# Kernel tuning notes

Hardware: AMD Instinct MI355X
Metric: run time of the kernel (lower is better)

Reference implementation:

```python
import jax, jax.numpy as jnp
import numpy as np

N = 50000      # nodes
E = 800000     # edges (avg degree 16)
IN_F = 128
HID = 128
NCLS = 64


def _lin(k, fi, fo):
    return jax.random.normal(k, (fi, fo), dtype=jnp.float32) / np.float32(np.sqrt(fi))


def setup_inputs() -> dict:
    key = jax.random.key(0)
    ks = jax.random.split(key, 10)
    features = jax.random.normal(ks[0], (N, IN_F), dtype=jnp.float32)
    noise = jax.random.normal(ks[1], (N, HID), dtype=jnp.float32)
    edge_src = jax.random.randint(ks[2], (E,), 0, N, dtype=jnp.int32)
    edge_dst = jax.random.randint(ks[3], (E,), 0, N, dtype=jnp.int32)
    Ws0 = _lin(ks[4], IN_F, HID); Wn0 = _lin(ks[5], IN_F, HID); b0 = jnp.zeros((HID,), jnp.float32)
    Ws1 = _lin(ks[6], HID, HID);  Wn1 = _lin(ks[7], HID, HID);  b1 = jnp.zeros((HID,), jnp.float32)
    Ws2 = _lin(ks[8], HID, NCLS); Wn2 = _lin(ks[9], HID, NCLS); b2 = jnp.zeros((NCLS,), jnp.float32)
    return dict(features=features, noise=noise,
                Ws0=Ws0, Wn0=Wn0, b0=b0,
                Ws1=Ws1, Wn1=Wn1, b1=b1,
                Ws2=Ws2, Wn2=Wn2, b2=b2,
                edge_src=edge_src, edge_dst=edge_dst, noise_d=1)


def _sage_layer(h, Ws, Wn, b, act, edge_src, edge_dst, deg_inv):
    # mean aggregation over incoming neighbors: gather src feats, segment-sum by dst
    msum = jax.ops.segment_sum(h[edge_src], edge_dst, num_segments=N)  # [N, F]
    h_neigh = msum * deg_inv[:, None]
    out = h @ Ws + h_neigh @ Wn + b
    return jax.nn.relu(out) if act else out


def reference(features, noise, Ws0, Wn0, b0, Ws1, Wn1, b1, Ws2, Wn2, b2,
              edge_src, edge_dst, noise_d):
    deg = jax.ops.segment_sum(jnp.ones((E,), jnp.float32), edge_dst, num_segments=N)
    deg_inv = 1.0 / jnp.maximum(deg, 1.0)
    layers = [(Ws0, Wn0, b0, True), (Ws1, Wn1, b1, True), (Ws2, Wn2, b2, False)]
    h = features
    h_noise = h
    for i, (Ws, Wn, b, act) in enumerate(layers):
        h = _sage_layer(h, Ws, Wn, b, act, edge_src, edge_dst, deg_inv)
        if noise_d == i:
            h_noise = h + noise
        if noise_d < i:
            h_noise = _sage_layer(h_noise, Ws, Wn, b, act, edge_src, edge_dst, deg_inv)
    return jnp.concatenate((h_noise, h), axis=1)  # [N, 2*NCLS]
```

## Files before the change

### kernel.cpp

```cpp
#include <hip/hip_runtime.h>

typedef __attribute__((ext_vector_type(8))) short bf16x8;
typedef __attribute__((ext_vector_type(4))) float f32x4;
typedef __attribute__((ext_vector_type(2))) float f32x2;

__device__ __forceinline__ unsigned short f2bf(float x) {
    union { float f; unsigned u; } v; v.f = x;
    unsigned r = v.u + 0x7FFFu + ((v.u >> 16) & 1u);
    return (unsigned short)(r >> 16);
}
__device__ __forceinline__ float bf2f(unsigned u) {
    union { unsigned u; float f; } v; v.u = u << 16;
    return v.f;
}
__device__ __forceinline__ unsigned char f2fp8(float x) {
    return (unsigned char)(__builtin_amdgcn_cvt_pk_fp8_f32(x, x, 0, false) & 0xff);
}

#define CHUNK 4096
#define CAP 4608

__global__ __launch_bounds__(256) void k_wt(
    const float* __restrict__ Ws0, const float* __restrict__ Wn0,
    const float* __restrict__ Ws1, const float* __restrict__ Wn1,
    const float* __restrict__ Ws2, const float* __restrict__ Wn2,
    unsigned short* __restrict__ WT0s, unsigned short* __restrict__ WT0n,
    unsigned short* __restrict__ WT1s, unsigned short* __restrict__ WT1n,
    unsigned short* __restrict__ WT2, int* __restrict__ bcursor) {
    int tid = threadIdx.x;
    if (blockIdx.x == 0) bcursor[tid] = 0;
    int i = blockIdx.x * 256 + tid;
    if (i < 16384)      { int j = i;         WT0s[j] = f2bf(Ws0[(j & 127) * 128 + (j >> 7)]); }
    else if (i < 32768) { int j = i - 16384; WT0n[j] = f2bf(Wn0[(j & 127) * 128 + (j >> 7)]); }
    else if (i < 49152) { int j = i - 32768; WT1s[j] = f2bf(Ws1[(j & 127) * 128 + (j >> 7)]); }
    else if (i < 65536) { int j = i - 49152; WT1n[j] = f2bf(Wn1[(j & 127) * 128 + (j >> 7)]); }
    else if (i < 73728) { int j = i - 65536; WT2[j] = f2bf(Ws2[(j & 127) * 64 + (j >> 7)]); }
    else if (i < 81920) { int j = i - 73728; WT2[8192 + j] = f2bf(Wn2[(j & 127) * 64 + (j >> 7)]); }
}

__global__ __launch_bounds__(256) void k_scatter_gemm0(
    const int* __restrict__ esrc, const int* __restrict__ edst,
    int* __restrict__ bcursor, unsigned* __restrict__ bsorted, int E, int ech,
    const float* __restrict__ Xf,
    const unsigned short* __restrict__ WsT, const unsigned short* __restrict__ WnT,
    const float* __restrict__ bias, unsigned short* __restrict__ Ab,
    unsigned char* __restrict__ T8, int N) {
    __shared__ uint4 smem[1216];
    int tid = threadIdx.x;
    if ((int)blockIdx.x < ech) {
        unsigned* stage = (unsigned*)smem;
        int* hist = (int*)(stage + CHUNK);
        int* base = hist + 256;
        int* cur  = base + 256;
        hist[tid] = 0;
        __syncthreads();
        int e0 = blockIdx.x * CHUNK;
        int cnt = min(CHUNK, E - e0);
        for (int i = tid; i < cnt; i += 256) {
            int d = edst[e0 + i], s = esrc[e0 + i];
            stage[i] = ((unsigned)d << 16) | (unsigned)s;
            atomicAdd(&hist[d >> 8], 1);
        }
        __syncthreads();
        int h = hist[tid];
        base[tid] = h ? (tid * CAP + atomicAdd(&bcursor[tid], h)) : 0;
        cur[tid] = 0;
        __syncthreads();
        for (int i = tid; i < cnt; i += 256) {
            unsigned pk = stage[i];
            int b = pk >> 24;
            int p = base[b] + atomicAdd(&cur[b], 1);
            bsorted[p] = pk;
        }
    } else {
        unsigned short (*xs)[136] = (unsigned short(*)[136])smem;
        int br = (blockIdx.x - ech) << 6;
        #pragma unroll
        for (int it = 0; it < 4; ++it) {
            int idx = tid + it * 256;
            int row = idx >> 4;
            int co = (idx & 15) << 3;
            int n = br + row;
            uint4 pk = make_uint4(0, 0, 0, 0);
            if (n < N) {
                float4 v0 = *(const float4*)(Xf + (size_t)n * 128 + co);
                float4 v1 = *(const float4*)(Xf + (size_t)n * 128 + co + 4);
                pk.x = (unsigned)f2bf(v0.x) | ((unsigned)f2bf(v0.y) << 16);
                pk.y = (unsigned)f2bf(v0.z) | ((unsigned)f2bf(v0.w) << 16);
                pk.z = (unsigned)f2bf(v1.x) | ((unsigned)f2bf(v1.y) << 16);
                pk.w = (unsigned)f2bf(v1.z) | ((unsigned)f2bf(v1.w) << 16);
            }
            *(uint4*)&xs[row][co] = pk;
        }
        __syncthreads();
        int wave = tid >> 6;
        int lane = tid & 63;
        int lrow = lane & 15;
        int kg = lane >> 4;
        int colbase = wave << 5;
        f32x4 acc[4][2][2];
        #pragma unroll
        for (int r = 0; r < 4; ++r)
            #pragma unroll
            for (int c = 0; c < 2; ++c) {
                acc[r][c][0] = (f32x4){0.f, 0.f, 0.f, 0.f};
                acc[r][c][1] = (f32x4){0.f, 0.f, 0.f, 0.f};
            }
        #pragma unroll
        for (int ks = 0; ks < 4; ++ks) {
            int kb = ks * 32 + kg * 8;
            bf16x8 af[4];
            #pragma unroll
            for (int r = 0; r < 4; ++r) af[r] = *(const bf16x8*)&xs[r * 16 + lrow][kb];
            bf16x8 bS[2], bN[2];
            #pragma unroll
            for (int c = 0; c < 2; ++c) {
                int col = colbase + c * 16 + lrow;
                bS[c] = *(const bf16x8*)(WsT + (size_t)col * 128 + kb);
                bN[c] = *(const bf16x8*)(WnT + (size_t)col * 128 + kb);
            }
            #pragma unroll
            for (int r = 0; r < 4; ++r)
                #pragma unroll
                for (int c = 0; c < 2; ++c) {
                    acc[r][c][0] = __builtin_amdgcn_mfma_f32_16x16x32_bf16(af[r], bS[c], acc[r][c][0], 0, 0, 0);
                    acc[r][c][1] = __builtin_amdgcn_mfma_f32_16x16x32_bf16(af[r], bN[c], acc[r][c][1], 0, 0, 0);
                }
        }
        #pragma unroll
        for (int r = 0; r < 4; ++r)
            #pragma unroll
            for (int c = 0; c < 2; ++c) {
                int col = colbase + c * 16 + lrow;
                float bv = bias[col];
                #pragma unroll
                for (int q = 0; q < 4; ++q) {
                    int n = br + r * 16 + kg * 4 + q;
                    if (n < N) {
                        Ab[(size_t)n * 128 + col] = f2bf(acc[r][c][0][q] + bv);
                        T8[(size_t)n * 128 + col] = f2fp8(acc[r][c][1][q]);
                    }
                }
            }
    }
}

__global__ __launch_bounds__(256) void k_bucket_csr(const unsigned* __restrict__ bsorted,
                                                    const int* __restrict__ bcursor,
                                                    int2* __restrict__ rbe,
                                                    float* __restrict__ dinv,
                                                    int* __restrict__ csr, int N) {
    __shared__ int sh[256];
    __shared__ int cur[256];
    int tid = threadIdx.x;
    int b = blockIdx.x;
    int lo = b * CAP;
    int hi = lo + bcursor[b];
    sh[tid] = 0;
    __syncthreads();
    for (int i = lo + tid; i < hi; i += 256) atomicAdd(&sh[(bsorted[i] >> 16) & 255], 1);
    __syncthreads();
    int v = sh[tid];
    __syncthreads();
    sh[tid] = v;
    __syncthreads();
    for (int off = 1; off < 256; off <<= 1) {
        int t = (tid >= off) ? sh[tid - off] : 0;
        __syncthreads();
        sh[tid] += t;
        __syncthreads();
    }
    int excl = sh[tid] - v;
    int d = (b << 8) + tid;
    if (d < N) {
        rbe[d] = make_int2(lo + excl, lo + excl + v);
        dinv[d] = 1.0f / (float)(v > 1 ? v : 1);
    }
    cur[tid] = lo + excl;
    __syncthreads();
    for (int i = lo + tid; i < hi; i += 256) {
        unsigned pk = bsorted[i];
        int p = atomicAdd(&cur[(pk >> 16) & 255], 1);
        csr[p] = (int)(pk & 0xffffu) << 6;
    }
}

__global__ __launch_bounds__(256) void k_mfma_dual(
    const unsigned short* __restrict__ Xin,
    const unsigned short* __restrict__ WsT, const unsigned short* __restrict__ WnT,
    const float* __restrict__ bias, unsigned short* __restrict__ Ab,
    unsigned char* __restrict__ T8, int N) {
    __shared__ unsigned short xs[64][136];
    int tid = threadIdx.x;
    int br = blockIdx.x << 6;
    #pragma unroll
    for (int it = 0; it < 4; ++it) {
        int idx = tid + it * 256;
        int row = idx >> 4;
        int co = (idx & 15) << 3;
        int n = br + row;
        uint4 pk = make_uint4(0, 0, 0, 0);
        if (n < N) pk = *(const uint4*)(Xin + (size_t)n * 128 + co);
        *(uint4*)&xs[row][co] = pk;
    }
    __syncthreads();
    int wave = tid >> 6;
    int lane = tid & 63;
    int lrow = lane & 15;
    int kg = lane >> 4;
    int colbase = wave << 5;
    f32x4 acc[4][2][2];
    #pragma unroll
    for (int r = 0; r < 4; ++r)
        #pragma unroll
        for (int c = 0; c < 2; ++c) {
            acc[r][c][0] = (f32x4){0.f, 0.f, 0.f, 0.f};
            acc[r][c][1] = (f32x4){0.f, 0.f, 0.f, 0.f};
        }
    #pragma unroll
    for (int ks = 0; ks < 4; ++ks) {
        int kb = ks * 32 + kg * 8;
        bf16x8 af[4];
        #pragma unroll
        for (int r = 0; r < 4; ++r) af[r] = *(const bf16x8*)&xs[r * 16 + lrow][kb];
        bf16x8 bS[2], bN[2];
        #pragma unroll
        for (int c = 0; c < 2; ++c) {
            int col = colbase + c * 16 + lrow;
            bS[c] = *(const bf16x8*)(WsT + (size_t)col * 128 + kb);
            bN[c] = *(const bf16x8*)(WnT + (size_t)col * 128 + kb);
        }
        #pragma unroll
        for (int r = 0; r < 4; ++r)
            #pragma unroll
            for (int c = 0; c < 2; ++c) {
                acc[r][c][0] = __builtin_amdgcn_mfma_f32_16x16x32_bf16(af[r], bS[c], acc[r][c][0], 0, 0, 0);
                acc[r][c][1] = __builtin_amdgcn_mfma_f32_16x16x32_bf16(af[r], bN[c], acc[r][c][1], 0, 0, 0);
            }
    }
    #pragma unroll
    for (int r = 0; r < 4; ++r)
        #pragma unroll
        for (int c = 0; c < 2; ++c) {
            int col = colbase + c * 16 + lrow;
            float bv = bias[col];
            #pragma unroll
            for (int q = 0; q < 4; ++q) {
                int n = br + r * 16 + kg * 4 + q;
                if (n < N) {
                    Ab[(size_t)n * 128 + col] = f2bf(acc[r][c][0][q] + bv);
                    T8[(size_t)n * 128 + col] = f2fp8(acc[r][c][1][q]);
                }
            }
        }
}

__global__ __launch_bounds__(256) void k_agg_relu(
    const unsigned short* __restrict__ T8p, const unsigned* __restrict__ Av,
    const float* __restrict__ dinv, const int2* __restrict__ rbe,
    const int* __restrict__ csr, unsigned* __restrict__ Hv, int N) {
    int w = (blockIdx.x * 256 + threadIdx.x) >> 6;
    int lane = threadIdx.x & 63;
    if (w >= N) return;
    int2 be = rbe[w];
    int e = be.x, ee = be.y;
    float ax = 0.f, ay = 0.f;
    for (; e + 16 <= ee; e += 16) {
        int o[16];
        #pragma unroll
        for (int j = 0; j < 16; ++j) o[j] = csr[e + j];
        unsigned short v[16];
        #pragma unroll
        for (int j = 0; j < 16; ++j) v[j] = T8p[(size_t)o[j] + lane];
        #pragma unroll
        for (int j = 0; j < 16; ++j) {
            f32x2 d = __builtin_amdgcn_cvt_pk_f32_fp8((unsigned)v[j], false);
            ax += d.x; ay += d.y;
        }
    }
    for (; e + 4 <= ee; e += 4) {
        int o[4];
        #pragma unroll
        for (int j = 0; j < 4; ++j) o[j] = csr[e + j];
        unsigned short v[4];
        #pragma unroll
        for (int j = 0; j < 4; ++j) v[j] = T8p[(size_t)o[j] + lane];
        #pragma unroll
        for (int j = 0; j < 4; ++j) {
            f32x2 d = __builtin_amdgcn_cvt_pk_f32_fp8((unsigned)v[j], false);
            ax += d.x; ay += d.y;
        }
    }
    for (; e < ee; ++e) {
        f32x2 d = __builtin_amdgcn_cvt_pk_f32_fp8((unsigned)T8p[(size_t)csr[e] + lane], false);
        ax += d.x; ay += d.y;
    }
    float di = dinv[w];
    unsigned av = Av[(size_t)w * 64 + lane];
    float ox = fmaxf(bf2f(av & 0xffff) + ax * di, 0.f);
    float oy = fmaxf(bf2f(av >> 16) + ay * di, 0.f);
    Hv[(size_t)w * 64 + lane] = (unsigned)f2bf(ox) | ((unsigned)f2bf(oy) << 16);
}

__global__ __launch_bounds__(256) void k_mfma_layer2(
    const unsigned short* __restrict__ Hb, const float* __restrict__ NZ,
    const unsigned short* __restrict__ WTcat, const float* __restrict__ b2,
    unsigned short* __restrict__ Sb, unsigned short* __restrict__ T8p, int N) {
    __shared__ unsigned short xh[64][136];
    __shared__ unsigned short xz[64][136];
    int tid = threadIdx.x;
    int br = blockIdx.x << 6;
    #pragma unroll
    for (int it = 0; it < 4; ++it) {
        int idx = tid + it * 256;
        int row = idx >> 4;
        int co = (idx & 15) << 3;
        int n = br + row;
        uint4 ph = make_uint4(0, 0, 0, 0), pz = make_uint4(0, 0, 0, 0);
        if (n < N) {
            ph = *(const uint4*)(Hb + (size_t)n * 128 + co);
            float4 v0 = *(const float4*)(NZ + (size_t)n * 128 + co);
            float4 v1 = *(const float4*)(NZ + (size_t)n * 128 + co + 4);
            pz.x = (unsigned)f2bf(v0.x) | ((unsigned)f2bf(v0.y) << 16);
            pz.y = (unsigned)f2bf(v0.z) | ((unsigned)f2bf(v0.w) << 16);
            pz.z = (unsigned)f2bf(v1.x) | ((unsigned)f2bf(v1.y) << 16);
            pz.w = (unsigned)f2bf(v1.z) | ((unsigned)f2bf(v1.w) << 16);
        }
        *(uint4*)&xh[row][co] = ph;
        *(uint4*)&xz[row][co] = pz;
    }
    __syncthreads();
    int wave = tid >> 6;
    int lane = tid & 63;
    int lrow = lane & 15;
    int kg = lane >> 4;
    int colbase = wave << 5;
    f32x4 acc[4][2][2];
    #pragma unroll
    for (int r = 0; r < 4; ++r)
        #pragma unroll
        for (int c = 0; c < 2; ++c) {
            acc[r][c][0] = (f32x4){0.f, 0.f, 0.f, 0.f};
            acc[r][c][1] = (f32x4){0.f, 0.f, 0.f, 0.f};
        }
    #pragma unroll
    for (int ks = 0; ks < 4; ++ks) {
        int kb = ks * 32 + kg * 8;
        bf16x8 ah[4], az[4];
        #pragma unroll
        for (int r = 0; r < 4; ++r) {
            ah[r] = *(const bf16x8*)&xh[r * 16 + lrow][kb];
            az[r] = *(const bf16x8*)&xz[r * 16 + lrow][kb];
        }
        bf16x8 bw[2];
        #pragma unroll
        for (int c = 0; c < 2; ++c) {
            int col = colbase + c * 16 + lrow;
            bw[c] = *(const bf16x8*)(WTcat + (size_t)col * 128 + kb);
        }
        #pragma unroll
        for (int r = 0; r < 4; ++r)
            #pragma unroll
            for (int c = 0; c < 2; ++c) {
                acc[r][c][0] = __builtin_amdgcn_mfma_f32_16x16x32_bf16(ah[r], bw[c], acc[r][c][0], 0, 0, 0);
                acc[r][c][1] = __builtin_amdgcn_mfma_f32_16x16x32_bf16(az[r], bw[c], acc[r][c][1], 0, 0, 0);
            }
    }
    if (wave < 2) {
        #pragma unroll
        for (int r = 0; r < 4; ++r)
            #pragma unroll
            for (int c = 0; c < 2; ++c) {
                int j = colbase + c * 16 + lrow;
                float bv = b2[j];
                #pragma unroll
                for (int q = 0; q < 4; ++q) {
                    int n = br + r * 16 + kg * 4 + q;
                    if (n < N) {
                        float hs = acc[r][c][0][q] + bv;
                        float zs = acc[r][c][1][q];
                        unsigned pk = (unsigned)f2bf(hs) | ((unsigned)f2bf(hs + zs) << 16);
                        ((unsigned*)Sb)[(size_t)n * 64 + j] = pk;
                    }
                }
            }
    } else {
        #pragma unroll
        for (int r = 0; r < 4; ++r)
            #pragma unroll
            for (int c = 0; c < 2; ++c) {
                int j = colbase - 64 + c * 16 + lrow;
                #pragma unroll
                for (int q = 0; q < 4; ++q) {
                    int n = br + r * 16 + kg * 4 + q;
                    if (n < N) {
                        unsigned pk = __builtin_amdgcn_cvt_pk_fp8_f32(
                            acc[r][c][0][q], acc[r][c][1][q], 0, false);
                        T8p[(size_t)n * 64 + j] = (unsigned short)(pk & 0xffffu);
                    }
                }
            }
    }
}

__global__ __launch_bounds__(256) void k_agg_final2(
    const unsigned short* __restrict__ T8p, const unsigned short* __restrict__ Sb,
    const float* __restrict__ dinv, const int2* __restrict__ rbe,
    const int* __restrict__ csr, float* __restrict__ out, int N) {
    int w = (blockIdx.x * 256 + threadIdx.x) >> 6;
    int lane = threadIdx.x & 63;
    if (w >= N) return;
    int2 be = rbe[w];
    int e = be.x, ee = be.y;
    float ax = 0.f, ay = 0.f;
    for (; e + 16 <= ee; e += 16) {
        int o[16];
        #pragma unroll
        for (int j = 0; j < 16; ++j) o[j] = csr[e + j];
        unsigned short v[16];
        #pragma unroll
        for (int j = 0; j < 16; ++j) v[j] = T8p[(size_t)o[j] + lane];
        #pragma unroll
        for (int j = 0; j < 16; ++j) {
            f32x2 d = __builtin_amdgcn_cvt_pk_f32_fp8((unsigned)v[j], false);
            ax += d.x; ay += d.y;
        }
    }
    for (; e + 4 <= ee; e += 4) {
        int o[4];
        #pragma unroll
        for (int j = 0; j < 4; ++j) o[j] = csr[e + j];
        unsigned short v[4];
        #pragma unroll
        for (int j = 0; j < 4; ++j) v[j] = T8p[(size_t)o[j] + lane];
        #pragma unroll
        for (int j = 0; j < 4; ++j) {
            f32x2 d = __builtin_amdgcn_cvt_pk_f32_fp8((unsigned)v[j], false);
            ax += d.x; ay += d.y;
        }
    }
    for (; e < ee; ++e) {
        f32x2 d = __builtin_amdgcn_cvt_pk_f32_fp8((unsigned)T8p[(size_t)csr[e] + lane], false);
        ax += d.x; ay += d.y;
    }
    float di = dinv[w];
    unsigned sv = ((const unsigned*)Sb)[(size_t)w * 64 + lane];
    float* orow = out + (size_t)w * 128;
    orow[64 + lane] = bf2f(sv & 0xffff) + ax * di;
    orow[lane]      = bf2f(sv >> 16) + (ax + ay) * di;
}

extern "C" void kernel_launch(void* const* d_in, const int* in_sizes, int n_in,
                              void* d_out, int out_size, void* d_ws, size_t ws_size,
                              hipStream_t stream) {
    const float* features = (const float*)d_in[0];
    const float* noise    = (const float*)d_in[1];
    const float* Ws0 = (const float*)d_in[2];
    const float* Wn0 = (const float*)d_in[3];
    const float* b0  = (const float*)d_in[4];
    const float* Ws1 = (const float*)d_in[5];
    const float* Wn1 = (const float*)d_in[6];
    const float* b1  = (const float*)d_in[7];
    const float* Ws2 = (const float*)d_in[8];
    const float* Wn2 = (const float*)d_in[9];
    const float* b2  = (const float*)d_in[10];
    const int* esrc = (const int*)d_in[11];
    const int* edst = (const int*)d_in[12];
    int N = in_sizes[0] / 128;
    int E = in_sizes[11];
    float* out = (float*)d_out;

    unsigned short* Ab = (unsigned short*)d_ws;
    unsigned short* Hb = Ab + (size_t)N * 128;
    unsigned short* Sb = Hb + (size_t)N * 128;
    unsigned char*  T8 = (unsigned char*)(Sb + (size_t)N * 128);
    unsigned short* WT0s = (unsigned short*)(T8 + (size_t)N * 128);
    unsigned short* WT0n = WT0s + 128 * 128;
    unsigned short* WT1s = WT0n + 128 * 128;
    unsigned short* WT1n = WT1s + 128 * 128;
    unsigned short* WT2  = WT1n + 128 * 128;
    float* dinv = (float*)(WT2 + 128 * 128);
    int2* rbe  = (int2*)(dinv + N);
    int* csr   = (int*)(rbe + N);
    unsigned* bsorted = (unsigned*)(csr + 256 * CAP);
    int* bcursor = (int*)(bsorted + 256 * CAP);

    int nbk = (N + 255) >> 8;
    int ech = (E + CHUNK - 1) / CHUNK;
    int g64 = (N + 63) / 64;

    k_wt<<<320, 256, 0, stream>>>(Ws0, Wn0, Ws1, Wn1, Ws2, Wn2,
                                  WT0s, WT0n, WT1s, WT1n, WT2, bcursor);
    k_scatter_gemm0<<<ech + g64, 256, 0, stream>>>(esrc, edst, bcursor, bsorted, E, ech,
                                                   features, WT0s, WT0n, b0, Ab, T8, N);
    k_bucket_csr<<<nbk, 256, 0, stream>>>(bsorted, bcursor, rbe, dinv, csr, N);

    int ablocks = (N * 64 + 255) / 256;

    k_agg_relu<<<ablocks, 256, 0, stream>>>((const unsigned short*)T8, (const unsigned*)Ab,
                                            dinv, rbe, csr, (unsigned*)Hb, N);
    k_mfma_dual<<<g64, 256, 0, stream>>>(Hb, WT1s, WT1n, b1, Ab, T8, N);
    k_agg_relu<<<ablocks, 256, 0, stream>>>((const unsigned short*)T8, (const unsigned*)Ab,
                                            dinv, rbe, csr, (unsigned*)Hb, N);
    k_mfma_layer2<<<g64, 256, 0, stream>>>(Hb, noise, WT2, b2, Sb, (unsigned short*)T8, N);
    k_agg_final2<<<ablocks, 256, 0, stream>>>((const unsigned short*)T8, Sb, dinv, rbe, csr, out, N);
}
```

Measured before the change: 180.9 us.

## Split each node's CSR neighbor list into four source-range segments

The bucket CSR build now counts edges per destination and per source quarter (src>>14), giving four sorted sub-ranges per node stored in a 4xN row-begin/end array. The aggregation kernels walk the four segments in order, so gathers run roughly in ascending source address within each quarter, aiming at better L2/TLB locality on the T8 feature gathers. This costs four rbe loads per node, a bigger workspace, and the 16-wide unrolled gather loop is dropped for 4-wide loops over shorter segments, which lowers memory-level parallelism.

```diff
diff --git a/kernel.cpp b/kernel.cpp
--- a/kernel.cpp
+++ b/kernel.cpp
@@ -150,38 +150,53 @@
                                                     int2* __restrict__ rbe,
                                                     float* __restrict__ dinv,
                                                     int* __restrict__ csr, int N) {
-    __shared__ int sh[256];
-    __shared__ int cur[256];
+    __shared__ int sh[1024];
+    __shared__ int cur[1024];
+    __shared__ int tsc[256];
     int tid = threadIdx.x;
     int b = blockIdx.x;
     int lo = b * CAP;
     int hi = lo + bcursor[b];
-    sh[tid] = 0;
-    __syncthreads();
-    for (int i = lo + tid; i < hi; i += 256) atomicAdd(&sh[(bsorted[i] >> 16) & 255], 1);
-    __syncthreads();
-    int v = sh[tid];
-    __syncthreads();
-    sh[tid] = v;
-    __syncthreads();
-    for (int off = 1; off < 256; off <<= 1) {
-        int t = (tid >= off) ? sh[tid - off] : 0;
-        __syncthreads();
-        sh[tid] += t;
-        __syncthreads();
-    }
-    int excl = sh[tid] - v;
-    int d = (b << 8) + tid;
-    if (d < N) {
-        rbe[d] = make_int2(lo + excl, lo + excl + v);
-        dinv[d] = 1.0f / (float)(v > 1 ? v : 1);
-    }
-    cur[tid] = lo + excl;
+    for (int i = tid; i < 1024; i += 256) sh[i] = 0;
     __syncthreads();
     for (int i = lo + tid; i < hi; i += 256) {
         unsigned pk = bsorted[i];
-        int p = atomicAdd(&cur[(pk >> 16) & 255], 1);
-        csr[p] = (int)(pk & 0xffffu) << 6;
+        int dl = (pk >> 16) & 255;
+        int seg = (pk & 0xffffu) >> 14;
+        atomicAdd(&sh[(dl << 2) | seg], 1);
+    }
+    __syncthreads();
+    int s0 = sh[tid * 4], s1 = sh[tid * 4 + 1], s2 = sh[tid * 4 + 2], s3 = sh[tid * 4 + 3];
+    int tsum = s0 + s1 + s2 + s3;
+    tsc[tid] = tsum;
+    __syncthreads();
+    for (int off = 1; off < 256; off <<= 1) {
+        int t = (tid >= off) ? tsc[tid - off] : 0;
+        __syncthreads();
+        tsc[tid] += t;
+        __syncthreads();
+    }
+    int p = tsc[tid] - tsum;
+    int e0 = p, e1 = p + s0, e2 = e1 + s1, e3 = e2 + s2;
+    cur[tid * 4]     = lo + e0;
+    cur[tid * 4 + 1] = lo + e1;
+    cur[tid * 4 + 2] = lo + e2;
+    cur[tid * 4 + 3] = lo + e3;
+    int d = (b << 8) + tid;
+    if (d < N) {
+        rbe[0 * (size_t)N + d] = make_int2(lo + e0, lo + e1);
+        rbe[1 * (size_t)N + d] = make_int2(lo + e1, lo + e2);
+        rbe[2 * (size_t)N + d] = make_int2(lo + e2, lo + e3);
+        rbe[3 * (size_t)N + d] = make_int2(lo + e3, lo + e3 + s3);
+        dinv[d] = 1.0f / (float)(tsum > 1 ? tsum : 1);
+    }
+    __syncthreads();
+    for (int i = lo + tid; i < hi; i += 256) {
+        unsigned pk = bsorted[i];
+        int dl = (pk >> 16) & 255;
+        int src = pk & 0xffffu;
+        int pp = atomicAdd(&cur[(dl << 2) | (src >> 14)], 1);
+        csr[pp] = src << 6;
     }
 }
 
@@ -262,38 +277,28 @@
     int w = (blockIdx.x * 256 + threadIdx.x) >> 6;
     int lane = threadIdx.x & 63;
     if (w >= N) return;
-    int2 be = rbe[w];
-    int e = be.x, ee = be.y;
     float ax = 0.f, ay = 0.f;
-    for (; e + 16 <= ee; e += 16) {
-        int o[16];
-        #pragma unroll
-        for (int j = 0; j < 16; ++j) o[j] = csr[e + j];
-        unsigned short v[16];
-        #pragma unroll
-        for (int j = 0; j < 16; ++j) v[j] = T8p[(size_t)o[j] + lane];
-        #pragma unroll
-        for (int j = 0; j < 16; ++j) {
-            f32x2 d = __builtin_amdgcn_cvt_pk_f32_fp8((unsigned)v[j], false);
+    #pragma unroll
+    for (int seg = 0; seg < 4; ++seg) {
+        int2 be = rbe[(size_t)seg * N + w];
+        int e = be.x, ee = be.y;
+        for (; e + 4 <= ee; e += 4) {
+            int o[4];
+            #pragma unroll
+            for (int j = 0; j < 4; ++j) o[j] = csr[e + j];
+            unsigned short v[4];
+            #pragma unroll
+            for (int j = 0; j < 4; ++j) v[j] = T8p[(size_t)o[j] + lane];
+            #pragma unroll
+            for (int j = 0; j < 4; ++j) {
+                f32x2 d = __builtin_amdgcn_cvt_pk_f32_fp8((unsigned)v[j], false);
+                ax += d.x; ay += d.y;
+            }
+        }
+        for (; e < ee; ++e) {
+            f32x2 d = __builtin_amdgcn_cvt_pk_f32_fp8((unsigned)T8p[(size_t)csr[e] + lane], false);
             ax += d.x; ay += d.y;
         }
-    }
-    for (; e + 4 <= ee; e += 4) {
-        int o[4];
-        #pragma unroll
-        for (int j = 0; j < 4; ++j) o[j] = csr[e + j];
-        unsigned short v[4];
-        #pragma unroll
-        for (int j = 0; j < 4; ++j) v[j] = T8p[(size_t)o[j] + lane];
-        #pragma unroll
-        for (int j = 0; j < 4; ++j) {
-            f32x2 d = __builtin_amdgcn_cvt_pk_f32_fp8((unsigned)v[j], false);
-            ax += d.x; ay += d.y;
-        }
-    }
-    for (; e < ee; ++e) {
-        f32x2 d = __builtin_amdgcn_cvt_pk_f32_fp8((unsigned)T8p[(size_t)csr[e] + lane], false);
-        ax += d.x; ay += d.y;
     }
     float di = dinv[w];
     unsigned av = Av[(size_t)w * 64 + lane];
@@ -410,38 +415,28 @@
     int w = (blockIdx.x * 256 + threadIdx.x) >> 6;
     int lane = threadIdx.x & 63;
     if (w >= N) return;
-    int2 be = rbe[w];
-    int e = be.x, ee = be.y;
     float ax = 0.f, ay = 0.f;
-    for (; e + 16 <= ee; e += 16) {
-        int o[16];
-        #pragma unroll
-        for (int j = 0; j < 16; ++j) o[j] = csr[e + j];
-        unsigned short v[16];
-        #pragma unroll
-        for (int j = 0; j < 16; ++j) v[j] = T8p[(size_t)o[j] + lane];
-        #pragma unroll
-        for (int j = 0; j < 16; ++j) {
-            f32x2 d = __builtin_amdgcn_cvt_pk_f32_fp8((unsigned)v[j], false);
+    #pragma unroll
+    for (int seg = 0; seg < 4; ++seg) {
+        int2 be = rbe[(size_t)seg * N + w];
+        int e = be.x, ee = be.y;
+        for (; e + 4 <= ee; e += 4) {
+            int o[4];
+            #pragma unroll
+            for (int j = 0; j < 4; ++j) o[j] = csr[e + j];
+            unsigned short v[4];
+            #pragma unroll
+            for (int j = 0; j < 4; ++j) v[j] = T8p[(size_t)o[j] + lane];
+            #pragma unroll
+            for (int j = 0; j < 4; ++j) {
+                f32x2 d = __builtin_amdgcn_cvt_pk_f32_fp8((unsigned)v[j], false);
+                ax += d.x; ay += d.y;
+            }
+        }
+        for (; e < ee; ++e) {
+            f32x2 d = __builtin_amdgcn_cvt_pk_f32_fp8((unsigned)T8p[(size_t)csr[e] + lane], false);
             ax += d.x; ay += d.y;
         }
-    }
-    for (; e + 4 <= ee; e += 4) {
-        int o[4];
-        #pragma unroll
-        for (int j = 0; j < 4; ++j) o[j] = csr[e + j];
-        unsigned short v[4];
-        #pragma unroll
-        for (int j = 0; j < 4; ++j) v[j] = T8p[(size_t)o[j] + lane];
-        #pragma unroll
-        for (int j = 0; j < 4; ++j) {
-            f32x2 d = __builtin_amdgcn_cvt_pk_f32_fp8((unsigned)v[j], false);
-            ax += d.x; ay += d.y;
-        }
-    }
-    for (; e < ee; ++e) {
-        f32x2 d = __builtin_amdgcn_cvt_pk_f32_fp8((unsigned)T8p[(size_t)csr[e] + lane], false);
-        ax += d.x; ay += d.y;
     }
     float di = dinv[w];
     unsigned sv = ((const unsigned*)Sb)[(size_t)w * 64 + lane];
@@ -481,7 +476,7 @@
     unsigned short* WT2  = WT1n + 128 * 128;
     float* dinv = (float*)(WT2 + 128 * 128);
     int2* rbe  = (int2*)(dinv + N);
-    int* csr   = (int*)(rbe + N);
+    int* csr   = (int*)(rbe + (size_t)4 * N);
     unsigned* bsorted = (unsigned*)(csr + 256 * CAP);
     int* bcursor = (int*)(bsorted + 256 * CAP);
 
```

Measured after the change: 240.8 us. 33.2% more time.

## Split fp8 neighbor table into two planar halves and aggregate with two waves per node

Applied to the files above, without the earlier changes.

The fp8 neighbor-projection tables become two column-half planes (N×64 bytes each) instead of one interleaved 128-byte row per node. The GEMM epilogues write to this layout. The aggregation kernels now launch one wave per (node, half), so each lane gathers one byte per edge instead of a 16-bit pair. This doubles the number of waves in flight to hide gather latency, at the cost of reading the CSR indices twice, narrower byte loads, and a lane shuffle in the final kernel to recombine the noise sum.

```diff
diff --git a/kernel.cpp b/kernel.cpp
--- a/kernel.cpp
+++ b/kernel.cpp
@@ -133,12 +133,13 @@
             for (int c = 0; c < 2; ++c) {
                 int col = colbase + c * 16 + lrow;
                 float bv = bias[col];
+                int hh = col >> 6, cl = col & 63;
                 #pragma unroll
                 for (int q = 0; q < 4; ++q) {
                     int n = br + r * 16 + kg * 4 + q;
                     if (n < N) {
                         Ab[(size_t)n * 128 + col] = f2bf(acc[r][c][0][q] + bv);
-                        T8[(size_t)n * 128 + col] = f2fp8(acc[r][c][1][q]);
+                        T8[((size_t)hh * N + n) * 64 + cl] = f2fp8(acc[r][c][1][q]);
                     }
                 }
             }
@@ -244,62 +245,53 @@
         for (int c = 0; c < 2; ++c) {
             int col = colbase + c * 16 + lrow;
             float bv = bias[col];
+            int hh = col >> 6, cl = col & 63;
             #pragma unroll
             for (int q = 0; q < 4; ++q) {
                 int n = br + r * 16 + kg * 4 + q;
                 if (n < N) {
                     Ab[(size_t)n * 128 + col] = f2bf(acc[r][c][0][q] + bv);
-                    T8[(size_t)n * 128 + col] = f2fp8(acc[r][c][1][q]);
+                    T8[((size_t)hh * N + n) * 64 + cl] = f2fp8(acc[r][c][1][q]);
                 }
             }
         }
 }
 
 __global__ __launch_bounds__(256) void k_agg_relu(
-    const unsigned short* __restrict__ T8p, const unsigned* __restrict__ Av,
+    const unsigned char* __restrict__ T8, const unsigned short* __restrict__ Ab,
     const float* __restrict__ dinv, const int2* __restrict__ rbe,
-    const int* __restrict__ csr, unsigned* __restrict__ Hv, int N) {
-    int w = (blockIdx.x * 256 + threadIdx.x) >> 6;
+    const int* __restrict__ csr, unsigned short* __restrict__ Hb, int N) {
+    int gw = (blockIdx.x * 256 + threadIdx.x) >> 6;
+    if (gw >= 2 * N) return;
+    int h = (gw >= N) ? 1 : 0;
+    int w = gw - h * N;
     int lane = threadIdx.x & 63;
-    if (w >= N) return;
+    const unsigned char* Tp = T8 + (size_t)h * N * 64;
     int2 be = rbe[w];
     int e = be.x, ee = be.y;
-    float ax = 0.f, ay = 0.f;
-    for (; e + 16 <= ee; e += 16) {
-        int o[16];
-        #pragma unroll
-        for (int j = 0; j < 16; ++j) o[j] = csr[e + j];
-        unsigned short v[16];
-        #pragma unroll
-        for (int j = 0; j < 16; ++j) v[j] = T8p[(size_t)o[j] + lane];
-        #pragma unroll
-        for (int j = 0; j < 16; ++j) {
+    float a = 0.f;
+    for (; e + 8 <= ee; e += 8) {
+        int o[8];
+        #pragma unroll
+        for (int j = 0; j < 8; ++j) o[j] = csr[e + j];
+        unsigned char v[8];
+        #pragma unroll
+        for (int j = 0; j < 8; ++j) v[j] = Tp[(size_t)o[j] + lane];
+        #pragma unroll
+        for (int j = 0; j < 8; ++j) {
             f32x2 d = __builtin_amdgcn_cvt_pk_f32_fp8((unsigned)v[j], false);
-            ax += d.x; ay += d.y;
-        }
-    }
-    for (; e + 4 <= ee; e += 4) {
-        int o[4];
-        #pragma unroll
-        for (int j = 0; j < 4; ++j) o[j] = csr[e + j];
-        unsigned short v[4];
-        #pragma unroll
-        for (int j = 0; j < 4; ++j) v[j] = T8p[(size_t)o[j] + lane];
-        #pragma unroll
-        for (int j = 0; j < 4; ++j) {
-            f32x2 d = __builtin_amdgcn_cvt_pk_f32_fp8((unsigned)v[j], false);
-            ax += d.x; ay += d.y;
+            a += d.x;
         }
     }
     for (; e < ee; ++e) {
-        f32x2 d = __builtin_amdgcn_cvt_pk_f32_fp8((unsigned)T8p[(size_t)csr[e] + lane], false);
-        ax += d.x; ay += d.y;
-    }
+        f32x2 d = __builtin_amdgcn_cvt_pk_f32_fp8((unsigned)Tp[(size_t)csr[e] + lane], false);
+        a += d.x;
+    }
+    int col = (h << 6) + lane;
     float di = dinv[w];
-    unsigned av = Av[(size_t)w * 64 + lane];
-    float ox = fmaxf(bf2f(av & 0xffff) + ax * di, 0.f);
-    float oy = fmaxf(bf2f(av >> 16) + ay * di, 0.f);
-    Hv[(size_t)w * 64 + lane] = (unsigned)f2bf(ox) | ((unsigned)f2bf(oy) << 16);
+    float aself = bf2f((unsigned)Ab[(size_t)w * 128 + col]);
+    float o = fmaxf(aself + a * di, 0.f);
+    Hb[(size_t)w * 128 + col] = f2bf(o);
 }
 
 __global__ __launch_bounds__(256) void k_mfma_layer2(
@@ -390,13 +382,14 @@
             #pragma unroll
             for (int c = 0; c < 2; ++c) {
                 int j = colbase - 64 + c * 16 + lrow;
+                int hh = j >> 5, jj = j & 31;
                 #pragma unroll
                 for (int q = 0; q < 4; ++q) {
                     int n = br + r * 16 + kg * 4 + q;
                     if (n < N) {
                         unsigned pk = __builtin_amdgcn_cvt_pk_fp8_f32(
                             acc[r][c][0][q], acc[r][c][1][q], 0, false);
-                        T8p[(size_t)n * 64 + j] = (unsigned short)(pk & 0xffffu);
+                        T8p[((size_t)hh * N + n) * 32 + jj] = (unsigned short)(pk & 0xffffu);
                     }
                 }
             }
@@ -404,50 +397,45 @@
 }
 
 __global__ __launch_bounds__(256) void k_agg_final2(
-    const unsigned short* __restrict__ T8p, const unsigned short* __restrict__ Sb,
+    const unsigned char* __restrict__ T8b, const unsigned short* __restrict__ Sb,
     const float* __restrict__ dinv, const int2* __restrict__ rbe,
     const int* __restrict__ csr, float* __restrict__ out, int N) {
-    int w = (blockIdx.x * 256 + threadIdx.x) >> 6;
+    int gw = (blockIdx.x * 256 + threadIdx.x) >> 6;
+    if (gw >= 2 * N) return;
+    int h = (gw >= N) ? 1 : 0;
+    int w = gw - h * N;
     int lane = threadIdx.x & 63;
-    if (w >= N) return;
+    const unsigned char* Tp = T8b + (size_t)h * N * 64;
     int2 be = rbe[w];
     int e = be.x, ee = be.y;
-    float ax = 0.f, ay = 0.f;
-    for (; e + 16 <= ee; e += 16) {
-        int o[16];
-        #pragma unroll
-        for (int j = 0; j < 16; ++j) o[j] = csr[e + j];
-        unsigned short v[16];
-        #pragma unroll
-        for (int j = 0; j < 16; ++j) v[j] = T8p[(size_t)o[j] + lane];
-        #pragma unroll
-        for (int j = 0; j < 16; ++j) {
+    float s = 0.f;
+    for (; e + 8 <= ee; e += 8) {
+        int o[8];
+        #pragma unroll
+        for (int j = 0; j < 8; ++j) o[j] = csr[e + j];
+        unsigned char v[8];
+        #pragma unroll
+        for (int j = 0; j < 8; ++j) v[j] = Tp[(size_t)o[j] + lane];
+        #pragma unroll
+        for (int j = 0; j < 8; ++j) {
             f32x2 d = __builtin_amdgcn_cvt_pk_f32_fp8((unsigned)v[j], false);
-            ax += d.x; ay += d.y;
-        }
-    }
-    for (; e + 4 <= ee; e += 4) {
-        int o[4];
-        #pragma unroll
-        for (int j = 0; j < 4; ++j) o[j] = csr[e + j];
-        unsigned short v[4];
-        #pragma unroll
-        for (int j = 0; j < 4; ++j) v[j] = T8p[(size_t)o[j] + lane];
-        #pragma unroll
-        for (int j = 0; j < 4; ++j) {
-            f32x2 d = __builtin_amdgcn_cvt_pk_f32_fp8((unsigned)v[j], false);
-            ax += d.x; ay += d.y;
+            s += d.x;
         }
     }
     for (; e < ee; ++e) {
-        f32x2 d = __builtin_amdgcn_cvt_pk_f32_fp8((unsigned)T8p[(size_t)csr[e] + lane], false);
-        ax += d.x; ay += d.y;
-    }
+        f32x2 d = __builtin_amdgcn_cvt_pk_f32_fp8((unsigned)Tp[(size_t)csr[e] + lane], false);
+        s += d.x;
+    }
+    float partner = __shfl_xor(s, 1, 64);
+    int col = (h << 5) + (lane >> 1);
     float di = dinv[w];
-    unsigned sv = ((const unsigned*)Sb)[(size_t)w * 64 + lane];
+    unsigned sv = ((const unsigned*)Sb)[(size_t)w * 64 + col];
     float* orow = out + (size_t)w * 128;
-    orow[64 + lane] = bf2f(sv & 0xffff) + ax * di;
-    orow[lane]      = bf2f(sv >> 16) + (ax + ay) * di;
+    if ((lane & 1) == 0) {
+        orow[64 + col] = bf2f(sv & 0xffff) + s * di;
+    } else {
+        orow[col] = bf2f(sv >> 16) + (partner + s) * di;
+    }
 }
 
 extern "C" void kernel_launch(void* const* d_in, const int* in_sizes, int n_in,
@@ -495,13 +483,11 @@
                                                    features, WT0s, WT0n, b0, Ab, T8, N);
     k_bucket_csr<<<nbk, 256, 0, stream>>>(bsorted, bcursor, rbe, dinv, csr, N);
 
-    int ablocks = (N * 64 + 255) / 256;
-
-    k_agg_relu<<<ablocks, 256, 0, stream>>>((const unsigned short*)T8, (const unsigned*)Ab,
-                                            dinv, rbe, csr, (unsigned*)Hb, N);
+    int ablocks = ((size_t)2 * N * 64 + 255) / 256;
+
+    k_agg_relu<<<ablocks, 256, 0, stream>>>(T8, Ab, dinv, rbe, csr, Hb, N);
     k_mfma_dual<<<g64, 256, 0, stream>>>(Hb, WT1s, WT1n, b1, Ab, T8, N);
-    k_agg_relu<<<ablocks, 256, 0, stream>>>((const unsigned short*)T8, (const unsigned*)Ab,
-                                            dinv, rbe, csr, (unsigned*)Hb, N);
+    k_agg_relu<<<ablocks, 256, 0, stream>>>(T8, Ab, dinv, rbe, csr, Hb, N);
     k_mfma_layer2<<<g64, 256, 0, stream>>>(Hb, noise, WT2, b2, Sb, (unsigned short*)T8, N);
-    k_agg_final2<<<ablocks, 256, 0, stream>>>((const unsigned short*)T8, Sb, dinv, rbe, csr, out, N);
-}
+    k_agg_final2<<<ablocks, 256, 0, stream>>>(T8, Sb, dinv, rbe, csr, out, N);
+}
```

Result: slower. 275.8 us (+52.5%).
